# Performance work log

Measured on AMD Instinct MI355X. Metric: run time of the kernel, lower is better.

The kernel has to match this reference:

```python
import jax, jax.numpy as jnp
import numpy as np

B, S, D = 2, 2048, 1024
H = 16
HD = D // H  # 64
THETA = 10000.0


def apply_rope(x, positions, theta):
    # x: (b, h, s, hd); positions: (s,)
    hd = x.shape[-1]
    inv_freq = theta ** (-jnp.arange(0, hd, 2, dtype=jnp.float32) / hd)  # (hd/2,)
    angles = positions.astype(jnp.float32)[:, None] * inv_freq[None, :]  # (s, hd/2)
    cos, sin = jnp.cos(angles), jnp.sin(angles)
    x1 = x[..., 0::2]
    x2 = x[..., 1::2]
    r1 = x1 * cos - x2 * sin
    r2 = x1 * sin + x2 * cos
    out = jnp.stack([r1, r2], axis=-1).reshape(x.shape)
    return out.astype(x.dtype)


def setup_inputs() -> dict:
    key = jax.random.key(0)
    ks = jax.random.split(key, 5)
    scale = 1.0 / np.sqrt(D)
    return {
        "in_features": jax.random.normal(ks[0], (B, S, D), dtype=jnp.float32),
        "token_positions": jnp.arange(S, dtype=jnp.int32),
        "Wq": jax.random.normal(ks[1], (D, D), dtype=jnp.float32) * scale,
        "Wk": jax.random.normal(ks[2], (D, D), dtype=jnp.float32) * scale,
        "Wv": jax.random.normal(ks[3], (D, D), dtype=jnp.float32) * scale,
        "Wo": jax.random.normal(ks[4], (D, D), dtype=jnp.float32) * scale,
    }


def reference(in_features, token_positions, Wq, Wk, Wv, Wo):
    b, s, d = in_features.shape
    h, hd = H, HD
    # bias-free linear: y = x @ W.T  (W is (out, in))
    q = in_features @ Wq.T
    k = in_features @ Wk.T
    v = in_features @ Wv.T
    # (b, s, h*hd) -> (b, h, s, hd)
    split = lambda t: t.reshape(b, s, h, hd).transpose(0, 2, 1, 3)
    q, k, v = split(q), split(k), split(v)
    q = apply_rope(q, token_positions, THETA)
    k = apply_rope(k, token_positions, THETA)
    scores = jnp.einsum("bhid,bhjd->bhij", q, k) / jnp.sqrt(jnp.asarray(hd, dtype=q.dtype))
    causal = jnp.triu(jnp.ones((s, s), dtype=bool), k=1)
    scores = jnp.where(causal, -jnp.inf, scores)
    attn = jax.nn.softmax(scores, axis=-1)
    out = jnp.einsum("bhij,bhjd->bhid", attn, v)
    out = out.transpose(0, 2, 1, 3).reshape(b, s, d)
    return out @ Wo.T
```

## Files before the change

kernel.cpp:

```cpp
#include <hip/hip_runtime.h>
#include <math.h>

#define NUM_HEADS 16
#define HEAD_DIM 64

typedef __bf16 bf16x8 __attribute__((ext_vector_type(8)));
typedef short shortx4 __attribute__((ext_vector_type(4)));
typedef float floatx4 __attribute__((ext_vector_type(4)));

__device__ __forceinline__ unsigned short f2b(float f) {
  unsigned int u = __float_as_uint(f);
  u += 0x7fffu + ((u >> 16) & 1u);
  return (unsigned short)(u >> 16);
}
__device__ __forceinline__ float b2f(unsigned short s) {
  return __uint_as_float(((unsigned int)s) << 16);
}

__device__ __forceinline__ void async16(const void* g, void* l) {
  __builtin_amdgcn_global_load_lds(
      (const __attribute__((address_space(1))) unsigned int*)g,
      (__attribute__((address_space(3))) unsigned int*)l, 16, 0, 0);
}

__global__ void cvt_f32_bf16(const float* __restrict__ in,
                             unsigned short* __restrict__ out, int n4) {
  int i = blockIdx.x * 256 + threadIdx.x;
  if (i < n4) {
    float4 v = ((const float4*)in)[i];
    ushort4 o;
    o.x = f2b(v.x); o.y = f2b(v.y); o.z = f2b(v.z); o.w = f2b(v.w);
    ((ushort4*)out)[i] = o;
  }
}

__global__ void cvt_w4(const float* __restrict__ w0, const float* __restrict__ w1,
                       const float* __restrict__ w2, const float* __restrict__ w3,
                       unsigned short* o0, unsigned short* o1,
                       unsigned short* o2, unsigned short* o3, int n4) {
  int i = blockIdx.x * 256 + threadIdx.x;
  if (i >= n4) return;
  const float* in = (blockIdx.y == 0) ? w0 : (blockIdx.y == 1) ? w1
                   : (blockIdx.y == 2) ? w2 : w3;
  unsigned short* out = (blockIdx.y == 0) ? o0 : (blockIdx.y == 1) ? o1
                       : (blockIdx.y == 2) ? o2 : o3;
  float4 v = ((const float4*)in)[i];
  ushort4 o;
  o.x = f2b(v.x); o.y = f2b(v.y); o.z = f2b(v.z); o.w = f2b(v.w);
  ((ushort4*)out)[i] = o;
}

__global__ void build_rope_tab(const int* __restrict__ pos,
                               float* __restrict__ tab, int total) {
  int t = blockIdx.x * 256 + threadIdx.x;
  if (t >= total) return;
  int i = t & 31, s = t >> 5;
  float inv = expf(-0.28782313662425575f * (float)i);
  float ang = (float)pos[s] * inv;
  float sn, cs;
  sincosf(ang, &sn, &cs);
  tab[t * 2] = cs;
  tab[t * 2 + 1] = sn;
}

template <int MODE>
__global__ __launch_bounds__(256, 2)
void gemm_bt(const unsigned short* __restrict__ A,
             const unsigned short* __restrict__ B0,
             const unsigned short* __restrict__ B1,
             const unsigned short* __restrict__ B2,
             void* out0v, void* out1v, void* out2v,
             const float* __restrict__ ctab,
             int M, int N, int K, int S) {
  __shared__ unsigned short As[128 * 32];
  __shared__ unsigned short Bs[128 * 32];
  const int tid = threadIdx.x;
  const int lane = tid & 63;
  const int w = tid >> 6;
  const int lane16 = lane & 15;
  const int g = lane >> 4;
  const int wm = w >> 1, wn = w & 1;
  const int m0 = blockIdx.y * 128;
  const int n0 = blockIdx.x * 128;
  const unsigned short* Bp = (blockIdx.z == 0) ? B0 : (blockIdx.z == 1 ? B1 : B2);

  const floatx4 vzero = {0.f, 0.f, 0.f, 0.f};
  floatx4 acc[4][4];
#pragma unroll
  for (int i = 0; i < 4; i++)
#pragma unroll
    for (int j = 0; j < 4; j++) acc[i][j] = vzero;

  const int ar = lane >> 2;
  const int ac = (lane & 3) * 8;

  for (int k0 = 0; k0 < K; k0 += 32) {
#pragma unroll
    for (int c = 0; c < 2; c++) {
      int chunk = w * 2 + c;
      async16(A  + (size_t)(m0 + chunk * 16 + ar) * K + k0 + ac, As + chunk * 512);
      async16(Bp + (size_t)(n0 + chunk * 16 + ar) * K + k0 + ac, Bs + chunk * 512);
    }
    __syncthreads();
    bf16x8 a[4], b[4];
#pragma unroll
    for (int mt = 0; mt < 4; mt++)
      a[mt] = *(const bf16x8*)&As[(wm * 64 + mt * 16 + lane16) * 32 + g * 8];
#pragma unroll
    for (int nt = 0; nt < 4; nt++)
      b[nt] = *(const bf16x8*)&Bs[(wn * 64 + nt * 16 + lane16) * 32 + g * 8];
#pragma unroll
    for (int mt = 0; mt < 4; mt++)
#pragma unroll
      for (int nt = 0; nt < 4; nt++)
        acc[mt][nt] = __builtin_amdgcn_mfma_f32_16x16x32_bf16(b[nt], a[mt], acc[mt][nt], 0, 0, 0);
    __syncthreads();
  }

  if (MODE == 0) {
    unsigned short* outp = (unsigned short*)((blockIdx.z == 0) ? out0v
                              : (blockIdx.z == 1 ? out1v : out2v));
    const bool dorope = (blockIdx.z < 2);
    const float qs = (blockIdx.z == 0) ? 0.125f : 1.0f;
#pragma unroll
    for (int mt = 0; mt < 4; mt++) {
      int m = m0 + wm * 64 + mt * 16 + lane16;
      int bb = m / S, s = m - bb * S;
      const float* crow = ctab + (size_t)s * 64;
#pragma unroll
      for (int nt = 0; nt < 4; nt++) {
        int n = n0 + wn * 64 + nt * 16 + g * 4;
        int h = n >> 6, dl = n & 63;
        floatx4 v = acc[mt][nt];
        if (dorope) {
          float4 cs = *(const float4*)&crow[dl];
          float r0 = (v[0] * cs.x - v[1] * cs.y) * qs;
          float r1 = (v[0] * cs.y + v[1] * cs.x) * qs;
          float r2 = (v[2] * cs.z - v[3] * cs.w) * qs;
          float r3 = (v[2] * cs.w + v[3] * cs.z) * qs;
          v[0] = r0; v[1] = r1; v[2] = r2; v[3] = r3;
        }
        shortx4 st;
#pragma unroll
        for (int r = 0; r < 4; r++) st[r] = (short)f2b(v[r]);
        *(shortx4*)&outp[(((size_t)(bb * NUM_HEADS + h) * S + s) << 6) + dl] = st;
      }
    }
  } else {
    float* outp = (float*)out0v;
#pragma unroll
    for (int mt = 0; mt < 4; mt++) {
      int m = m0 + wm * 64 + mt * 16 + lane16;
#pragma unroll
      for (int nt = 0; nt < 4; nt++) {
        int n = n0 + wn * 64 + nt * 16 + g * 4;
        *(floatx4*)&outp[(size_t)m * N + n] = acc[mt][nt];
      }
    }
  }
}

__global__ __launch_bounds__(256, 4)
void transpose_v(const unsigned short* __restrict__ V,
                 unsigned short* __restrict__ Vt, int S) {
  __shared__ unsigned short t[64 * 72];
  const int tid = threadIdx.x;
  const int lane = tid & 63;
  const int w = tid >> 6;
  const int bh = blockIdx.y;
  const int s0 = blockIdx.x * 64;
  const size_t ibase = (size_t)bh * S * 64;
#pragma unroll
  for (int c = 0; c < 2; ++c) {
    int ch = c * 4 + w;
    union { uint4 v; unsigned short u[8]; } vb;
    vb.v = *(const uint4*)&V[ibase + (size_t)(s0 + lane) * 64 + ch * 8];
#pragma unroll
    for (int e = 0; e < 8; ++e) t[(ch * 8 + e) * 72 + lane] = vb.u[e];
  }
  __syncthreads();
  const size_t obase = (size_t)bh * 64 * S;
#pragma unroll
  for (int c = 0; c < 2; ++c) {
    int idx = c * 256 + tid;
    int d = idx >> 3, sch = idx & 7;
    *(uint4*)&Vt[obase + (size_t)d * S + s0 + sch * 8] = *(const uint4*)&t[d * 72 + sch * 8];
  }
}

__global__ __launch_bounds__(256, 4)
void flash_attn4(const unsigned short* __restrict__ Q,
                 const unsigned short* __restrict__ Kv,
                 const unsigned short* __restrict__ Vt,
                 unsigned short* __restrict__ Oattn, int S) {
  __shared__ unsigned short Ks[2 * 4096];
  __shared__ unsigned short Vs[2 * 4096];
  const int tid = threadIdx.x;
  const int lane = tid & 63;
  const int w = tid >> 6;
  const int lane16 = lane & 15;
  const int g = lane >> 4;
  const int sw = lane16 & 7;
  const int qt = gridDim.x - 1 - blockIdx.x;
  const int bh = blockIdx.y;
  const int b = bh >> 4, h = bh & 15;
  const size_t kbase = (size_t)bh * S * HEAD_DIM;
  const unsigned short* Kbase = Kv + kbase;
  const unsigned short* Vtbase = Vt + (size_t)bh * HEAD_DIM * S;
  const int qrow0 = qt * 64 + w * 16;

  bf16x8 qf0, qf1;
  {
    const unsigned short* qp = Q + kbase + (size_t)(qrow0 + lane16) * HEAD_DIM + g * 8;
    qf0 = *(const bf16x8*)qp;
    qf1 = *(const bf16x8*)(qp + 32);
  }

  const int ci0 = w * 64 + lane;
  const int ci1 = ci0 + 256;
  const int r0 = ci0 >> 3, j0 = (ci0 & 7) ^ (r0 & 7);
  const int r1 = ci1 >> 3, j1 = (ci1 & 7) ^ (r1 & 7);
  const unsigned short* kS0 = Kbase + r0 * HEAD_DIM + j0 * 8;
  const unsigned short* kS1 = Kbase + r1 * HEAD_DIM + j1 * 8;
  const unsigned short* vS0 = Vtbase + (size_t)r0 * S + j0 * 8;
  const unsigned short* vS1 = Vtbase + (size_t)r1 * S + j1 * 8;
  unsigned short* kD0 = Ks + ci0 * 8;
  unsigned short* kD1 = Ks + ci1 * 8;
  unsigned short* vD0 = Vs + ci0 * 8;
  unsigned short* vD1 = Vs + ci1 * 8;

  auto stage = [&](int t, int bi) {
    int koff = t * 4096;
    int voff = t * 64;
    int doff = bi * 4096;
    async16(kS0 + koff, kD0 + doff);
    async16(kS1 + koff, kD1 + doff);
    async16(vS0 + voff, vD0 + doff);
    async16(vS1 + voff, vD1 + doff);
  };

  const floatx4 vzero = {0.f, 0.f, 0.f, 0.f};
  floatx4 oacc[4];
#pragma unroll
  for (int i = 0; i < 4; i++) oacc[i] = vzero;
  float l_i = 0.f;

  stage(0, 0);
  __syncthreads();

  for (int t = 0; t <= qt; ++t) {
    const int bi = t & 1;
    if (t < qt) stage(t + 1, bi ^ 1);
    const unsigned short* Kb_ = Ks + bi * 4096;
    const unsigned short* Vb_ = Vs + bi * 4096;

    floatx4 sc[4];
#pragma unroll
    for (int c = 0; c < 4; ++c) {
      int r = c * 16 + lane16;
      bf16x8 kf0 = *(const bf16x8*)&Kb_[(r * 8 + (g ^ sw)) * 8];
      bf16x8 kf1 = *(const bf16x8*)&Kb_[(r * 8 + ((4 + g) ^ sw)) * 8];
      floatx4 s = vzero;
      s = __builtin_amdgcn_mfma_f32_16x16x32_bf16(kf0, qf0, s, 0, 0, 0);
      s = __builtin_amdgcn_mfma_f32_16x16x32_bf16(kf1, qf1, s, 0, 0, 0);
      sc[c] = s;
    }
    if (t == qt) {
      const int i = qrow0 + lane16;
      const int jb = t * 64;
#pragma unroll
      for (int c = 0; c < 4; ++c)
#pragma unroll
        for (int r = 0; r < 4; ++r)
          if (jb + c * 16 + g * 4 + r > i) sc[c][r] = -INFINITY;
    }
    shortx4 pc[4];
#pragma unroll
    for (int c = 0; c < 4; ++c) {
      float p0 = __expf(sc[c][0]);
      float p1 = __expf(sc[c][1]);
      float p2 = __expf(sc[c][2]);
      float p3 = __expf(sc[c][3]);
      l_i += (p0 + p1) + (p2 + p3);
      union { unsigned int u[2]; shortx4 s4; } pu;
      pu.u[0] = __builtin_amdgcn_perm(__float_as_uint(p1), __float_as_uint(p0), 0x07060302u);
      pu.u[1] = __builtin_amdgcn_perm(__float_as_uint(p3), __float_as_uint(p2), 0x07060302u);
      pc[c] = pu.s4;
    }
#pragma unroll
    for (int nt = 0; nt < 4; ++nt) {
      int rv = nt * 16 + lane16;
#pragma unroll
      for (int c = 0; c < 4; ++c) {
        shortx4 vf = *(const shortx4*)&Vb_[(rv * 8 + ((c * 2 + (g >> 1)) ^ sw)) * 8 + (g & 1) * 4];
        oacc[nt] = __builtin_amdgcn_mfma_f32_16x16x16bf16_1k(vf, pc[c], oacc[nt], 0, 0, 0);
      }
    }
    __syncthreads();
  }

  l_i += __shfl_xor(l_i, 16, 64);
  l_i += __shfl_xor(l_i, 32, 64);
  {
    float inv = 1.0f / l_i;
    int srow = qrow0 + lane16;
    size_t rowb = ((size_t)b * S + srow) * 1024 + h * 64;
#pragma unroll
    for (int nt = 0; nt < 4; ++nt) {
      shortx4 st;
#pragma unroll
      for (int r = 0; r < 4; ++r) st[r] = (short)f2b(oacc[nt][r] * inv);
      *(shortx4*)&Oattn[rowb + nt * 16 + g * 4] = st;
    }
  }
}

extern "C" void kernel_launch(void* const* d_in, const int* in_sizes, int n_in,
                              void* d_out, int out_size, void* d_ws, size_t ws_size,
                              hipStream_t stream) {
  const float* x  = (const float*)d_in[0];
  const int*  pos = (const int*)d_in[1];
  const float* wq = (const float*)d_in[2];
  const float* wk = (const float*)d_in[3];
  const float* wv = (const float*)d_in[4];
  const float* wo = (const float*)d_in[5];

  const int D = 1024;
  const int S = in_sizes[1];
  const int M = in_sizes[0] / D;
  const int B = M / S;
  const int BH = B * NUM_HEADS;

  char* wsb = (char*)d_ws;
  size_t off = 0;
  auto alloc = [&](size_t bytes) {
    char* p = wsb + off;
    off += (bytes + 255) & ~(size_t)255;
    return p;
  };
  unsigned short* Xb   = (unsigned short*)alloc((size_t)M * D * 2);
  unsigned short* Wqb  = (unsigned short*)alloc((size_t)D * D * 2);
  unsigned short* Wkb  = (unsigned short*)alloc((size_t)D * D * 2);
  unsigned short* Wvb  = (unsigned short*)alloc((size_t)D * D * 2);
  unsigned short* Wob  = (unsigned short*)alloc((size_t)D * D * 2);
  unsigned short* Qb   = (unsigned short*)alloc((size_t)M * D * 2);
  unsigned short* Kb   = (unsigned short*)alloc((size_t)M * D * 2);
  unsigned short* Vb   = (unsigned short*)alloc((size_t)M * D * 2);
  unsigned short* Attn = (unsigned short*)alloc((size_t)M * D * 2);
  float*          Ctab = (float*)alloc((size_t)S * 32 * 2 * 4);
  unsigned short* Vtb  = Xb;
  (void)ws_size;

  {
    int n4 = M * D / 4;
    cvt_f32_bf16<<<dim3((n4 + 255) / 256), 256, 0, stream>>>(x, Xb, n4);
    int w4 = D * D / 4;
    cvt_w4<<<dim3((w4 + 255) / 256, 4), 256, 0, stream>>>(
        wq, wk, wv, wo, Wqb, Wkb, Wvb, Wob, w4);
    int tt = S * 32;
    build_rope_tab<<<dim3((tt + 255) / 256), 256, 0, stream>>>(pos, Ctab, tt);
  }
  gemm_bt<0><<<dim3(D / 128, M / 128, 3), 256, 0, stream>>>(
      Xb, Wqb, Wkb, Wvb, Qb, Kb, Vb, Ctab, M, D, D, S);
  transpose_v<<<dim3(S / 64, BH), 256, 0, stream>>>(Vb, Vtb, S);
  flash_attn4<<<dim3(S / 64, BH), 256, 0, stream>>>(Qb, Kb, Vtb, Attn, S);
  gemm_bt<1><<<dim3(D / 128, M / 128, 1), 256, 0, stream>>>(
      Attn, Wob, Wob, Wob, d_out, d_out, d_out, Ctab, M, D, D, S);
}
```

Measured before the change: 204.2 us.

## Double-buffer GEMM K-tiles and process two query tiles per attention block

The projection GEMM now double-buffers its A/B shared-memory tiles so the next K slice loads asynchronously while the current one is computed, dropping one barrier per iteration. The flash-attention kernel now handles 128 query rows per block (two 16-row slices per wave), reusing each loaded K/V tile for twice as many queries and halving the grid. This cuts global K/V traffic and barrier overhead, but raises register use (launch bounds lowered to 2) and halves the number of blocks, which may reduce occupancy and worsen load balance across the causal triangle.

```diff
diff --git a/kernel.cpp b/kernel.cpp
--- a/kernel.cpp
+++ b/kernel.cpp
@@ -12,9 +12,6 @@
   unsigned int u = __float_as_uint(f);
   u += 0x7fffu + ((u >> 16) & 1u);
   return (unsigned short)(u >> 16);
-}
-__device__ __forceinline__ float b2f(unsigned short s) {
-  return __uint_as_float(((unsigned int)s) << 16);
 }
 
 __device__ __forceinline__ void async16(const void* g, void* l) {
@@ -72,8 +69,8 @@
              void* out0v, void* out1v, void* out2v,
              const float* __restrict__ ctab,
              int M, int N, int K, int S) {
-  __shared__ unsigned short As[128 * 32];
-  __shared__ unsigned short Bs[128 * 32];
+  __shared__ unsigned short As[2 * 4096];
+  __shared__ unsigned short Bs[2 * 4096];
   const int tid = threadIdx.x;
   const int lane = tid & 63;
   const int w = tid >> 6;
@@ -93,22 +90,38 @@
 
   const int ar = lane >> 2;
   const int ac = (lane & 3) * 8;
+  const unsigned short* aS0 = A  + (size_t)(m0 + (w * 2 + 0) * 16 + ar) * K + ac;
+  const unsigned short* aS1 = A  + (size_t)(m0 + (w * 2 + 1) * 16 + ar) * K + ac;
+  const unsigned short* bS0 = Bp + (size_t)(n0 + (w * 2 + 0) * 16 + ar) * K + ac;
+  const unsigned short* bS1 = Bp + (size_t)(n0 + (w * 2 + 1) * 16 + ar) * K + ac;
+  unsigned short* aD0 = As + (w * 2 + 0) * 512;
+  unsigned short* aD1 = As + (w * 2 + 1) * 512;
+  unsigned short* bD0 = Bs + (w * 2 + 0) * 512;
+  unsigned short* bD1 = Bs + (w * 2 + 1) * 512;
+
+  auto stage = [&](int k0, int bi) {
+    int doff = bi * 4096;
+    async16(aS0 + k0, aD0 + doff);
+    async16(aS1 + k0, aD1 + doff);
+    async16(bS0 + k0, bD0 + doff);
+    async16(bS1 + k0, bD1 + doff);
+  };
+
+  stage(0, 0);
+  __syncthreads();
 
   for (int k0 = 0; k0 < K; k0 += 32) {
-#pragma unroll
-    for (int c = 0; c < 2; c++) {
-      int chunk = w * 2 + c;
-      async16(A  + (size_t)(m0 + chunk * 16 + ar) * K + k0 + ac, As + chunk * 512);
-      async16(Bp + (size_t)(n0 + chunk * 16 + ar) * K + k0 + ac, Bs + chunk * 512);
-    }
-    __syncthreads();
+    const int bi = (k0 >> 5) & 1;
+    if (k0 + 32 < K) stage(k0 + 32, bi ^ 1);
+    const unsigned short* Ab = As + bi * 4096;
+    const unsigned short* Bb = Bs + bi * 4096;
     bf16x8 a[4], b[4];
 #pragma unroll
     for (int mt = 0; mt < 4; mt++)
-      a[mt] = *(const bf16x8*)&As[(wm * 64 + mt * 16 + lane16) * 32 + g * 8];
+      a[mt] = *(const bf16x8*)&Ab[(wm * 64 + mt * 16 + lane16) * 32 + g * 8];
 #pragma unroll
     for (int nt = 0; nt < 4; nt++)
-      b[nt] = *(const bf16x8*)&Bs[(wn * 64 + nt * 16 + lane16) * 32 + g * 8];
+      b[nt] = *(const bf16x8*)&Bb[(wn * 64 + nt * 16 + lane16) * 32 + g * 8];
 #pragma unroll
     for (int mt = 0; mt < 4; mt++)
 #pragma unroll
@@ -188,8 +201,8 @@
   }
 }
 
-__global__ __launch_bounds__(256, 4)
-void flash_attn4(const unsigned short* __restrict__ Q,
+__global__ __launch_bounds__(256, 2)
+void flash_attn5(const unsigned short* __restrict__ Q,
                  const unsigned short* __restrict__ Kv,
                  const unsigned short* __restrict__ Vt,
                  unsigned short* __restrict__ Oattn, int S) {
@@ -201,19 +214,23 @@
   const int lane16 = lane & 15;
   const int g = lane >> 4;
   const int sw = lane16 & 7;
-  const int qt = gridDim.x - 1 - blockIdx.x;
+  const int qb = gridDim.x - 1 - blockIdx.x;
   const int bh = blockIdx.y;
   const int b = bh >> 4, h = bh & 15;
   const size_t kbase = (size_t)bh * S * HEAD_DIM;
   const unsigned short* Kbase = Kv + kbase;
   const unsigned short* Vtbase = Vt + (size_t)bh * HEAD_DIM * S;
-  const int qrow0 = qt * 64 + w * 16;
-
-  bf16x8 qf0, qf1;
-  {
-    const unsigned short* qp = Q + kbase + (size_t)(qrow0 + lane16) * HEAD_DIM + g * 8;
-    qf0 = *(const bf16x8*)qp;
-    qf1 = *(const bf16x8*)(qp + 32);
+  const int base0 = qb * 128 + w * 16;
+  const int base1 = base0 + 64;
+  const int tmax = 2 * qb + 1;
+
+  bf16x8 qf[2][2];
+#pragma unroll
+  for (int s = 0; s < 2; ++s) {
+    const unsigned short* qp =
+        Q + kbase + (size_t)(base0 + s * 64 + lane16) * HEAD_DIM + g * 8;
+    qf[s][0] = *(const bf16x8*)qp;
+    qf[s][1] = *(const bf16x8*)(qp + 32);
   }
 
   const int ci0 = w * 64 + lane;
@@ -240,76 +257,95 @@
   };
 
   const floatx4 vzero = {0.f, 0.f, 0.f, 0.f};
-  floatx4 oacc[4];
-#pragma unroll
-  for (int i = 0; i < 4; i++) oacc[i] = vzero;
-  float l_i = 0.f;
+  floatx4 oacc[2][4];
+#pragma unroll
+  for (int s = 0; s < 2; ++s)
+#pragma unroll
+    for (int i = 0; i < 4; i++) oacc[s][i] = vzero;
+  float l_i[2] = {0.f, 0.f};
 
   stage(0, 0);
   __syncthreads();
 
-  for (int t = 0; t <= qt; ++t) {
+  for (int t = 0; t <= tmax; ++t) {
     const int bi = t & 1;
-    if (t < qt) stage(t + 1, bi ^ 1);
+    if (t < tmax) stage(t + 1, bi ^ 1);
     const unsigned short* Kb_ = Ks + bi * 4096;
     const unsigned short* Vb_ = Vs + bi * 4096;
 
-    floatx4 sc[4];
+    floatx4 sc[2][4];
 #pragma unroll
     for (int c = 0; c < 4; ++c) {
       int r = c * 16 + lane16;
       bf16x8 kf0 = *(const bf16x8*)&Kb_[(r * 8 + (g ^ sw)) * 8];
       bf16x8 kf1 = *(const bf16x8*)&Kb_[(r * 8 + ((4 + g) ^ sw)) * 8];
-      floatx4 s = vzero;
-      s = __builtin_amdgcn_mfma_f32_16x16x32_bf16(kf0, qf0, s, 0, 0, 0);
-      s = __builtin_amdgcn_mfma_f32_16x16x32_bf16(kf1, qf1, s, 0, 0, 0);
-      sc[c] = s;
-    }
-    if (t == qt) {
-      const int i = qrow0 + lane16;
+      floatx4 s0 = vzero, s1 = vzero;
+      s0 = __builtin_amdgcn_mfma_f32_16x16x32_bf16(kf0, qf[0][0], s0, 0, 0, 0);
+      s1 = __builtin_amdgcn_mfma_f32_16x16x32_bf16(kf0, qf[1][0], s1, 0, 0, 0);
+      s0 = __builtin_amdgcn_mfma_f32_16x16x32_bf16(kf1, qf[0][1], s0, 0, 0, 0);
+      s1 = __builtin_amdgcn_mfma_f32_16x16x32_bf16(kf1, qf[1][1], s1, 0, 0, 0);
+      sc[0][c] = s0;
+      sc[1][c] = s1;
+    }
+    if (t >= tmax - 1) {
+      const int i0 = base0 + lane16;
       const int jb = t * 64;
 #pragma unroll
       for (int c = 0; c < 4; ++c)
 #pragma unroll
         for (int r = 0; r < 4; ++r)
-          if (jb + c * 16 + g * 4 + r > i) sc[c][r] = -INFINITY;
-    }
-    shortx4 pc[4];
-#pragma unroll
-    for (int c = 0; c < 4; ++c) {
-      float p0 = __expf(sc[c][0]);
-      float p1 = __expf(sc[c][1]);
-      float p2 = __expf(sc[c][2]);
-      float p3 = __expf(sc[c][3]);
-      l_i += (p0 + p1) + (p2 + p3);
-      union { unsigned int u[2]; shortx4 s4; } pu;
-      pu.u[0] = __builtin_amdgcn_perm(__float_as_uint(p1), __float_as_uint(p0), 0x07060302u);
-      pu.u[1] = __builtin_amdgcn_perm(__float_as_uint(p3), __float_as_uint(p2), 0x07060302u);
-      pc[c] = pu.s4;
-    }
+          if (jb + c * 16 + g * 4 + r > i0) sc[0][c][r] = -INFINITY;
+    }
+    if (t == tmax) {
+      const int i1 = base1 + lane16;
+      const int jb = t * 64;
+#pragma unroll
+      for (int c = 0; c < 4; ++c)
+#pragma unroll
+        for (int r = 0; r < 4; ++r)
+          if (jb + c * 16 + g * 4 + r > i1) sc[1][c][r] = -INFINITY;
+    }
+    shortx4 pc[2][4];
+#pragma unroll
+    for (int s = 0; s < 2; ++s)
+#pragma unroll
+      for (int c = 0; c < 4; ++c) {
+        float p0 = __expf(sc[s][c][0]);
+        float p1 = __expf(sc[s][c][1]);
+        float p2 = __expf(sc[s][c][2]);
+        float p3 = __expf(sc[s][c][3]);
+        l_i[s] += (p0 + p1) + (p2 + p3);
+        union { unsigned int u[2]; shortx4 s4; } pu;
+        pu.u[0] = __builtin_amdgcn_perm(__float_as_uint(p1), __float_as_uint(p0), 0x07060302u);
+        pu.u[1] = __builtin_amdgcn_perm(__float_as_uint(p3), __float_as_uint(p2), 0x07060302u);
+        pc[s][c] = pu.s4;
+      }
 #pragma unroll
     for (int nt = 0; nt < 4; ++nt) {
       int rv = nt * 16 + lane16;
 #pragma unroll
       for (int c = 0; c < 4; ++c) {
         shortx4 vf = *(const shortx4*)&Vb_[(rv * 8 + ((c * 2 + (g >> 1)) ^ sw)) * 8 + (g & 1) * 4];
-        oacc[nt] = __builtin_amdgcn_mfma_f32_16x16x16bf16_1k(vf, pc[c], oacc[nt], 0, 0, 0);
+        oacc[0][nt] = __builtin_amdgcn_mfma_f32_16x16x16bf16_1k(vf, pc[0][c], oacc[0][nt], 0, 0, 0);
+        oacc[1][nt] = __builtin_amdgcn_mfma_f32_16x16x16bf16_1k(vf, pc[1][c], oacc[1][nt], 0, 0, 0);
       }
     }
     __syncthreads();
   }
 
-  l_i += __shfl_xor(l_i, 16, 64);
-  l_i += __shfl_xor(l_i, 32, 64);
-  {
-    float inv = 1.0f / l_i;
-    int srow = qrow0 + lane16;
+#pragma unroll
+  for (int s = 0; s < 2; ++s) {
+    float l = l_i[s];
+    l += __shfl_xor(l, 16, 64);
+    l += __shfl_xor(l, 32, 64);
+    float inv = 1.0f / l;
+    int srow = base0 + s * 64 + lane16;
     size_t rowb = ((size_t)b * S + srow) * 1024 + h * 64;
 #pragma unroll
     for (int nt = 0; nt < 4; ++nt) {
       shortx4 st;
 #pragma unroll
-      for (int r = 0; r < 4; ++r) st[r] = (short)f2b(oacc[nt][r] * inv);
+      for (int r = 0; r < 4; ++r) st[r] = (short)f2b(oacc[s][nt][r] * inv);
       *(shortx4*)&Oattn[rowb + nt * 16 + g * 4] = st;
     }
   }
@@ -363,7 +399,7 @@
   gemm_bt<0><<<dim3(D / 128, M / 128, 3), 256, 0, stream>>>(
       Xb, Wqb, Wkb, Wvb, Qb, Kb, Vb, Ctab, M, D, D, S);
   transpose_v<<<dim3(S / 64, BH), 256, 0, stream>>>(Vb, Vtb, S);
-  flash_attn4<<<dim3(S / 64, BH), 256, 0, stream>>>(Qb, Kb, Vtb, Attn, S);
+  flash_attn5<<<dim3(S / 128, BH), 256, 0, stream>>>(Qb, Kb, Vtb, Attn, S);
   gemm_bt<1><<<dim3(D / 128, M / 128, 1), 256, 0, stream>>>(
       Attn, Wob, Wob, Wob, d_out, d_out, d_out, Ctab, M, D, D, S);
 }
```

Measured after the change: 210.0 us. 2.9% more time.

## Pre-pack K/V into MFMA fragment order and double-buffer GEMM LDS tiles

Applied to the files above, without the earlier changes.

Attention no longer stages K/V tiles through LDS. A new pack_kv kernel rewrites K and V in place into per-lane MFMA fragment order, so flash attention loads operands straight from global memory into registers with coalesced loads and no block barriers. The projection GEMM gains double-buffered LDS staging that prefetches the next K-slice while the current one computes, and the occupancy hint rises to 3 blocks. The risk is that attention now depends on L2/global latency instead of shared-memory reuse across the four waves, and the larger LDS footprint may limit GEMM occupancy.

```diff
diff --git a/kernel.cpp b/kernel.cpp
--- a/kernel.cpp
+++ b/kernel.cpp
@@ -12,9 +12,6 @@
   unsigned int u = __float_as_uint(f);
   u += 0x7fffu + ((u >> 16) & 1u);
   return (unsigned short)(u >> 16);
-}
-__device__ __forceinline__ float b2f(unsigned short s) {
-  return __uint_as_float(((unsigned int)s) << 16);
 }
 
 __device__ __forceinline__ void async16(const void* g, void* l) {
@@ -64,7 +61,7 @@
 }
 
 template <int MODE>
-__global__ __launch_bounds__(256, 2)
+__global__ __launch_bounds__(256, 3)
 void gemm_bt(const unsigned short* __restrict__ A,
              const unsigned short* __restrict__ B0,
              const unsigned short* __restrict__ B1,
@@ -72,8 +69,8 @@
              void* out0v, void* out1v, void* out2v,
              const float* __restrict__ ctab,
              int M, int N, int K, int S) {
-  __shared__ unsigned short As[128 * 32];
-  __shared__ unsigned short Bs[128 * 32];
+  __shared__ unsigned short As[2 * 4096];
+  __shared__ unsigned short Bs[2 * 4096];
   const int tid = threadIdx.x;
   const int lane = tid & 63;
   const int w = tid >> 6;
@@ -93,28 +90,45 @@
 
   const int ar = lane >> 2;
   const int ac = (lane & 3) * 8;
+  const unsigned short* aS0 = A  + (size_t)(m0 + (w * 2 + 0) * 16 + ar) * K + ac;
+  const unsigned short* aS1 = A  + (size_t)(m0 + (w * 2 + 1) * 16 + ar) * K + ac;
+  const unsigned short* bS0 = Bp + (size_t)(n0 + (w * 2 + 0) * 16 + ar) * K + ac;
+  const unsigned short* bS1 = Bp + (size_t)(n0 + (w * 2 + 1) * 16 + ar) * K + ac;
+  unsigned short* aD0 = As + (w * 2 + 0) * 512;
+  unsigned short* aD1 = As + (w * 2 + 1) * 512;
+  unsigned short* bD0 = Bs + (w * 2 + 0) * 512;
+  unsigned short* bD1 = Bs + (w * 2 + 1) * 512;
+
+  auto stage = [&](int k0, int bi) {
+    int doff = bi * 4096;
+    async16(aS0 + k0, aD0 + doff);
+    async16(aS1 + k0, aD1 + doff);
+    async16(bS0 + k0, bD0 + doff);
+    async16(bS1 + k0, bD1 + doff);
+  };
+
+  stage(0, 0);
+  __syncthreads();
 
   for (int k0 = 0; k0 < K; k0 += 32) {
-#pragma unroll
-    for (int c = 0; c < 2; c++) {
-      int chunk = w * 2 + c;
-      async16(A  + (size_t)(m0 + chunk * 16 + ar) * K + k0 + ac, As + chunk * 512);
-      async16(Bp + (size_t)(n0 + chunk * 16 + ar) * K + k0 + ac, Bs + chunk * 512);
-    }
-    __syncthreads();
+    const int bi = (k0 >> 5) & 1;
+    if (k0 + 32 < K) stage(k0 + 32, bi ^ 1);
+    const unsigned short* Ab = As + bi * 4096;
+    const unsigned short* Bb = Bs + bi * 4096;
     bf16x8 a[4], b[4];
 #pragma unroll
     for (int mt = 0; mt < 4; mt++)
-      a[mt] = *(const bf16x8*)&As[(wm * 64 + mt * 16 + lane16) * 32 + g * 8];
+      a[mt] = *(const bf16x8*)&Ab[(wm * 64 + mt * 16 + lane16) * 32 + g * 8];
 #pragma unroll
     for (int nt = 0; nt < 4; nt++)
-      b[nt] = *(const bf16x8*)&Bs[(wn * 64 + nt * 16 + lane16) * 32 + g * 8];
+      b[nt] = *(const bf16x8*)&Bs[bi * 4096 + (wn * 64 + nt * 16 + lane16) * 32 + g * 8];
 #pragma unroll
     for (int mt = 0; mt < 4; mt++)
 #pragma unroll
       for (int nt = 0; nt < 4; nt++)
         acc[mt][nt] = __builtin_amdgcn_mfma_f32_16x16x32_bf16(b[nt], a[mt], acc[mt][nt], 0, 0, 0);
     __syncthreads();
+    (void)Bb;
   }
 
   if (MODE == 0) {
@@ -161,105 +175,83 @@
 }
 
 __global__ __launch_bounds__(256, 4)
-void transpose_v(const unsigned short* __restrict__ V,
-                 unsigned short* __restrict__ Vt, int S) {
-  __shared__ unsigned short t[64 * 72];
+void pack_kv(unsigned short* __restrict__ K, unsigned short* __restrict__ V,
+             int S) {
+  __shared__ unsigned short Kl[64 * 72];
+  __shared__ unsigned short Vl[64 * 72];
   const int tid = threadIdx.x;
   const int lane = tid & 63;
   const int w = tid >> 6;
-  const int bh = blockIdx.y;
-  const int s0 = blockIdx.x * 64;
-  const size_t ibase = (size_t)bh * S * 64;
+  const int t = blockIdx.x, bh = blockIdx.y;
+  const size_t base = ((size_t)bh * (S >> 6) + t) * 4096;
+#pragma unroll
+  for (int c = 0; c < 2; ++c) {
+    int idx = c * 256 + tid;
+    int row = idx >> 3, ch = idx & 7;
+    *(uint4*)&Kl[row * 72 + ch * 8] = *(const uint4*)&K[base + row * 64 + ch * 8];
+  }
 #pragma unroll
   for (int c = 0; c < 2; ++c) {
     int ch = c * 4 + w;
     union { uint4 v; unsigned short u[8]; } vb;
-    vb.v = *(const uint4*)&V[ibase + (size_t)(s0 + lane) * 64 + ch * 8];
-#pragma unroll
-    for (int e = 0; e < 8; ++e) t[(ch * 8 + e) * 72 + lane] = vb.u[e];
+    vb.v = *(const uint4*)&V[base + lane * 64 + ch * 8];
+#pragma unroll
+    for (int e = 0; e < 8; ++e) Vl[(ch * 8 + e) * 72 + lane] = vb.u[e];
   }
   __syncthreads();
-  const size_t obase = (size_t)bh * 64 * S;
 #pragma unroll
   for (int c = 0; c < 2; ++c) {
-    int idx = c * 256 + tid;
-    int d = idx >> 3, sch = idx & 7;
-    *(uint4*)&Vt[obase + (size_t)d * S + s0 + sch * 8] = *(const uint4*)&t[d * 72 + sch * 8];
+    int f = w * 2 + c;
+    int jt = f >> 1, half = f & 1;
+    uint4 d = *(const uint4*)&Kl[(jt * 16 + (lane & 15)) * 72 + half * 32 + (lane >> 4) * 8];
+    *(uint4*)&K[base + f * 512 + lane * 8] = d;
+  }
+#pragma unroll
+  for (int nt = 0; nt < 4; ++nt) {
+    uint2 d = *(const uint2*)&Vl[(nt * 16 + (lane & 15)) * 72 + w * 16 + (lane >> 4) * 4];
+    *(uint2*)&V[base + (w * 4 + nt) * 256 + lane * 4] = d;
   }
 }
 
 __global__ __launch_bounds__(256, 4)
-void flash_attn4(const unsigned short* __restrict__ Q,
-                 const unsigned short* __restrict__ Kv,
-                 const unsigned short* __restrict__ Vt,
+void flash_attn6(const unsigned short* __restrict__ Q,
+                 const unsigned short* __restrict__ Kp,
+                 const unsigned short* __restrict__ Vp,
                  unsigned short* __restrict__ Oattn, int S) {
-  __shared__ unsigned short Ks[2 * 4096];
-  __shared__ unsigned short Vs[2 * 4096];
   const int tid = threadIdx.x;
   const int lane = tid & 63;
   const int w = tid >> 6;
   const int lane16 = lane & 15;
   const int g = lane >> 4;
-  const int sw = lane16 & 7;
   const int qt = gridDim.x - 1 - blockIdx.x;
   const int bh = blockIdx.y;
   const int b = bh >> 4, h = bh & 15;
-  const size_t kbase = (size_t)bh * S * HEAD_DIM;
-  const unsigned short* Kbase = Kv + kbase;
-  const unsigned short* Vtbase = Vt + (size_t)bh * HEAD_DIM * S;
+  const size_t hb = (size_t)bh * S * HEAD_DIM;
   const int qrow0 = qt * 64 + w * 16;
 
   bf16x8 qf0, qf1;
   {
-    const unsigned short* qp = Q + kbase + (size_t)(qrow0 + lane16) * HEAD_DIM + g * 8;
+    const unsigned short* qp = Q + hb + (size_t)(qrow0 + lane16) * HEAD_DIM + g * 8;
     qf0 = *(const bf16x8*)qp;
     qf1 = *(const bf16x8*)(qp + 32);
   }
-
-  const int ci0 = w * 64 + lane;
-  const int ci1 = ci0 + 256;
-  const int r0 = ci0 >> 3, j0 = (ci0 & 7) ^ (r0 & 7);
-  const int r1 = ci1 >> 3, j1 = (ci1 & 7) ^ (r1 & 7);
-  const unsigned short* kS0 = Kbase + r0 * HEAD_DIM + j0 * 8;
-  const unsigned short* kS1 = Kbase + r1 * HEAD_DIM + j1 * 8;
-  const unsigned short* vS0 = Vtbase + (size_t)r0 * S + j0 * 8;
-  const unsigned short* vS1 = Vtbase + (size_t)r1 * S + j1 * 8;
-  unsigned short* kD0 = Ks + ci0 * 8;
-  unsigned short* kD1 = Ks + ci1 * 8;
-  unsigned short* vD0 = Vs + ci0 * 8;
-  unsigned short* vD1 = Vs + ci1 * 8;
-
-  auto stage = [&](int t, int bi) {
-    int koff = t * 4096;
-    int voff = t * 64;
-    int doff = bi * 4096;
-    async16(kS0 + koff, kD0 + doff);
-    async16(kS1 + koff, kD1 + doff);
-    async16(vS0 + voff, vD0 + doff);
-    async16(vS1 + voff, vD1 + doff);
-  };
-
   const floatx4 vzero = {0.f, 0.f, 0.f, 0.f};
   floatx4 oacc[4];
 #pragma unroll
   for (int i = 0; i < 4; i++) oacc[i] = vzero;
   float l_i = 0.f;
 
-  stage(0, 0);
-  __syncthreads();
+  const unsigned short* kb = Kp + hb + lane * 8;
+  const unsigned short* vb = Vp + hb + lane * 4;
 
   for (int t = 0; t <= qt; ++t) {
-    const int bi = t & 1;
-    if (t < qt) stage(t + 1, bi ^ 1);
-    const unsigned short* Kb_ = Ks + bi * 4096;
-    const unsigned short* Vb_ = Vs + bi * 4096;
-
+    const unsigned short* kt = kb + t * 4096;
+    const unsigned short* vt = vb + t * 4096;
     floatx4 sc[4];
 #pragma unroll
     for (int c = 0; c < 4; ++c) {
-      int r = c * 16 + lane16;
-      bf16x8 kf0 = *(const bf16x8*)&Kb_[(r * 8 + (g ^ sw)) * 8];
-      bf16x8 kf1 = *(const bf16x8*)&Kb_[(r * 8 + ((4 + g) ^ sw)) * 8];
+      bf16x8 kf0 = *(const bf16x8*)&kt[(c * 2 + 0) * 512];
+      bf16x8 kf1 = *(const bf16x8*)&kt[(c * 2 + 1) * 512];
       floatx4 s = vzero;
       s = __builtin_amdgcn_mfma_f32_16x16x32_bf16(kf0, qf0, s, 0, 0, 0);
       s = __builtin_amdgcn_mfma_f32_16x16x32_bf16(kf1, qf1, s, 0, 0, 0);
@@ -288,15 +280,12 @@
       pc[c] = pu.s4;
     }
 #pragma unroll
-    for (int nt = 0; nt < 4; ++nt) {
-      int rv = nt * 16 + lane16;
+    for (int nt = 0; nt < 4; ++nt)
 #pragma unroll
       for (int c = 0; c < 4; ++c) {
-        shortx4 vf = *(const shortx4*)&Vb_[(rv * 8 + ((c * 2 + (g >> 1)) ^ sw)) * 8 + (g & 1) * 4];
+        shortx4 vf = *(const shortx4*)&vt[(c * 4 + nt) * 256];
         oacc[nt] = __builtin_amdgcn_mfma_f32_16x16x16bf16_1k(vf, pc[c], oacc[nt], 0, 0, 0);
       }
-    }
-    __syncthreads();
   }
 
   l_i += __shfl_xor(l_i, 16, 64);
@@ -348,7 +337,6 @@
   unsigned short* Vb   = (unsigned short*)alloc((size_t)M * D * 2);
   unsigned short* Attn = (unsigned short*)alloc((size_t)M * D * 2);
   float*          Ctab = (float*)alloc((size_t)S * 32 * 2 * 4);
-  unsigned short* Vtb  = Xb;
   (void)ws_size;
 
   {
@@ -362,8 +350,8 @@
   }
   gemm_bt<0><<<dim3(D / 128, M / 128, 3), 256, 0, stream>>>(
       Xb, Wqb, Wkb, Wvb, Qb, Kb, Vb, Ctab, M, D, D, S);
-  transpose_v<<<dim3(S / 64, BH), 256, 0, stream>>>(Vb, Vtb, S);
-  flash_attn4<<<dim3(S / 64, BH), 256, 0, stream>>>(Qb, Kb, Vtb, Attn, S);
+  pack_kv<<<dim3(S / 64, BH), 256, 0, stream>>>(Kb, Vb, S);
+  flash_attn6<<<dim3(S / 64, BH), 256, 0, stream>>>(Qb, Kb, Vb, Attn, S);
   gemm_bt<1><<<dim3(D / 128, M / 128, 1), 256, 0, stream>>>(
       Attn, Wob, Wob, Wob, d_out, d_out, d_out, Ctab, M, D, D, S);
 }
```

New measurement: 252.7 us. 23.8% more time.
